# Optimization experiments

Measured on AMD Instinct MI355X. Metric: run time of the kernel, lower is better.

Reference implementation:

```python
import jax, jax.numpy as jnp
import numpy as np

N = 50000
E = 800000
IN = 128
C = 32   # out_channels per head
H = 4    # heads
HC = H * C
EDGE_DIM = 1
NEG_SLOPE = 0.2
BN_EPS = 1e-5


def setup_inputs() -> dict:
    key = jax.random.key(0)
    ks = jax.random.split(key, 12)
    glorot = lambda k, shp: (jax.random.uniform(k, shp, jnp.float32, -1.0, 1.0)
                             * jnp.sqrt(6.0 / (shp[0] + shp[-1])))
    return {
        "x": jax.random.normal(ks[0], (N, IN), jnp.float32),
        "edge_index": jax.random.randint(ks[1], (2, E), 0, N, jnp.int64),
        "edge_attr": jax.random.normal(ks[2], (E, EDGE_DIM), jnp.float32),
        # GATv2Conv params
        "W_l": glorot(ks[3], (IN, HC)),   # lin_l (source)
        "b_l": jnp.zeros((HC,), jnp.float32),
        "W_r": glorot(ks[4], (IN, HC)),   # lin_r (target)
        "b_r": jnp.zeros((HC,), jnp.float32),
        "W_e": glorot(ks[5], (EDGE_DIM, HC)),  # lin_edge (no bias)
        "att": glorot(ks[6], (H, C)),
        "bias": jnp.zeros((HC,), jnp.float32),  # final conv bias (concat)
        # BatchNorm1d affine params
        "gamma": jnp.ones((HC,), jnp.float32),
        "beta": jnp.zeros((HC,), jnp.float32),
    }


def reference(x, edge_index, edge_attr, W_l, b_l, W_r, b_r, W_e, att, bias, gamma, beta):
    src = edge_index[0]  # message source j
    dst = edge_index[1]  # message target i (aggregation segment)

    x_l = (x @ W_l + b_l).reshape(N, H, C)  # source transform
    x_r = (x @ W_r + b_r).reshape(N, H, C)  # target transform
    e = (edge_attr @ W_e).reshape(E, H, C)  # edge transform

    # GATv2 attention: LeakyReLU(x_i + x_j + e) . att, per edge & head
    m = jax.nn.leaky_relu(x_l[src] + x_r[dst] + e, NEG_SLOPE)  # [E,H,C]
    alpha = jnp.einsum('ehc,hc->eh', m, att)                   # [E,H]

    # segment softmax over destination nodes (numerically stable)
    amax = jax.ops.segment_max(alpha, dst, num_segments=N)     # [N,H]
    ex = jnp.exp(alpha - amax[dst])
    denom = jax.ops.segment_sum(ex, dst, num_segments=N)       # [N,H]
    alpha = ex / (denom[dst] + 1e-16)

    # scatter-add aggregation of weighted source features
    out = jax.ops.segment_sum(x_l[src] * alpha[:, :, None], dst, num_segments=N)
    out = out.reshape(N, HC) + bias

    # BatchNorm1d (training-mode batch statistics), then ELU; dropout = eval (identity)
    mean = out.mean(axis=0)
    var = out.var(axis=0)
    out = (out - mean) * jax.lax.rsqrt(var + BN_EPS) * gamma + beta
    return jax.nn.elu(out)
```

## Files before the change

kernel.cpp:

```cpp
#include <hip/hip_runtime.h>
#include <math.h>

constexpr int NN  = 50000;
constexpr int NE  = 800000;
constexpr int IND = 128;
constexpr int HCD = 128;

constexpr int NBKT = 250;
constexpr int NPB  = 200;
constexpr int BCAP = 4096;
constexpr int BE   = 2048;
constexpr int EPT  = BE / 256;
constexpr int B1B  = (NE + BE - 1) / BE;

constexpr int BM = 128;
constexpr int BK = 32;
constexpr int GTILES = (NN + BM - 1) / BM;

typedef __attribute__((ext_vector_type(8))) short bf16x8;
typedef __attribute__((ext_vector_type(4))) float f32x4;
typedef __attribute__((ext_vector_type(2))) float f32x2;

__device__ __forceinline__ void splitbf(float f, unsigned short &h, unsigned short &lo) {
    unsigned u = __float_as_uint(f);
    h = (unsigned short)(u >> 16);
    float fh = __uint_as_float(u & 0xffff0000u);
    lo = (unsigned short)(__float_as_uint(f - fh) >> 16);
}
__device__ __forceinline__ unsigned short bf16rne(float f) {
    unsigned u = __float_as_uint(f);
    u += 0x7fffu + ((u >> 16) & 1u);
    return (unsigned short)(u >> 16);
}

template<int CTRL>
__device__ __forceinline__ float dpp_qadd(float p) {
    int t = __builtin_amdgcn_mov_dpp(__float_as_int(p), CTRL, 0xF, 0xF, true);
    return p + __int_as_float(t);
}

__global__ __launch_bounds__(256) void gemm_bucket(
    const float* __restrict__ x, const float* __restrict__ Wl,
    const float* __restrict__ Wr, const float* __restrict__ bl,
    const float* __restrict__ br, unsigned short* __restrict__ xlbf,
    unsigned short* __restrict__ xrbf,
    const int* __restrict__ src, const int* __restrict__ dst,
    const float* __restrict__ ea, int* __restrict__ gcur,
    int2* __restrict__ stg)
{
    extern __shared__ char smem[];
    const int tid = threadIdx.x;

    if (blockIdx.x < B1B) {
        int2* sedge = (int2*)smem;
        int*  cnt   = (int*)(smem + 16384);
        int*  lofs  = (int*)(smem + 17408);
        int*  gbase = (int*)(smem + 18432);
        int*  tsc   = (int*)(smem + 19456);

        for (int j = tid; j < NBKT; j += 256) cnt[j] = 0;
        __syncthreads();

        const int e0 = blockIdx.x * BE;
        unsigned w0[EPT]; int w1[EPT]; int nb[EPT];
#pragma unroll
        for (int j = 0; j < EPT; ++j) {
            int e = e0 + j * 256 + tid;
            bool ok = e < NE;
            int s_ = ok ? src[e] : 0;
            int d_ = ok ? dst[e] : 0;
            float a_ = ok ? ea[e] : 0.f;
            int b  = d_ / NPB;
            int dl = d_ - b * NPB;
            w0[j] = (unsigned)s_ | ((unsigned)dl << 16) | ((unsigned)b << 24);
            w1[j] = __float_as_int(a_);
            nb[j] = ok ? b : -1;
            if (ok) atomicAdd(&cnt[b], 1);
        }
        __syncthreads();
        int v = (tid < NBKT) ? cnt[tid] : 0;
        tsc[tid] = v;
        __syncthreads();
        for (int d = 1; d < 256; d <<= 1) {
            int u = (tid >= d) ? tsc[tid - d] : 0;
            __syncthreads();
            tsc[tid] += u;
            __syncthreads();
        }
        if (tid < NBKT) {
            lofs[tid]  = tsc[tid] - v;
            gbase[tid] = v ? atomicAdd(&gcur[tid], v) : 0;
            cnt[tid]   = 0;
        }
        __syncthreads();
#pragma unroll
        for (int j = 0; j < EPT; ++j) {
            if (nb[j] >= 0) {
                int slot = lofs[nb[j]] + atomicAdd(&cnt[nb[j]], 1);
                sedge[slot] = make_int2((int)w0[j], w1[j]);
            }
        }
        __syncthreads();
        const int total = min(NE - e0, BE);
        for (int idx = tid; idx < total; idx += 256) {
            int2 v2 = sedge[idx];
            int b = ((unsigned)v2.x) >> 24;
            int gpos = gbase[b] + (idx - lofs[b]);
            if (gpos < BCAP)
                stg[b * BCAP + gpos] = v2;
        }
        return;
    }

    char* Ah = smem;
    char* Al = smem + 8192;
    char* Bh = smem + 16384;

    const int bblk = blockIdx.x - B1B;
    const int side = bblk & 1;
    const float* W  = side ? Wr : Wl;
    const float* bv = side ? br : bl;
    unsigned short* outp = side ? xrbf : xlbf;
    const int bn = (bblk >> 1) * BM;

    const int l   = tid & 63;
    const int wid = tid >> 6;
    const int wr  = (wid >> 1) * 64;
    const int wc  = (wid & 1) * 64;
    const int lr  = l & 15;
    const int kg  = l >> 4;

    f32x4 acc[4][4];
#pragma unroll
    for (int s = 0; s < 4; ++s)
#pragma unroll
        for (int f = 0; f < 4; ++f) acc[s][f] = (f32x4){0.f, 0.f, 0.f, 0.f};

    const int cB  = tid & 127;
    const int khB = tid >> 7;

    for (int ki = 0; ki < 4; ++ki) {
#pragma unroll
        for (int r = 0; r < 4; ++r) {
            int g = tid + r * 256;
            int row = g >> 3, k4 = g & 7;
            int node = bn + row;
            float4 v = make_float4(0.f, 0.f, 0.f, 0.f);
            if (node < NN) v = *(const float4*)&x[node * IND + ki * BK + k4 * 4];
            unsigned short h0, h1, h2, h3, q0, q1, q2, q3;
            splitbf(v.x, h0, q0); splitbf(v.y, h1, q1);
            splitbf(v.z, h2, q2); splitbf(v.w, h3, q3);
            int off = (row * BK + k4 * 4) * 2;
            int swz = off ^ ((row & 7) << 4);
            *(ushort4*)(Ah + swz) = make_ushort4(h0, h1, h2, h3);
            *(ushort4*)(Al + swz) = make_ushort4(q0, q1, q2, q3);
        }
#pragma unroll
        for (int r = 0; r < 4; ++r) {
            int kb = r * 8 + khB * 4;
            float f0 = W[(ki * BK + kb + 0) * HCD + cB];
            float f1 = W[(ki * BK + kb + 1) * HCD + cB];
            float f2 = W[(ki * BK + kb + 2) * HCD + cB];
            float f3 = W[(ki * BK + kb + 3) * HCD + cB];
            int off = (cB * BK + kb) * 2;
            int swz = off ^ ((cB & 7) << 4);
            *(ushort4*)(Bh + swz) = make_ushort4(bf16rne(f0), bf16rne(f1),
                                                 bf16rne(f2), bf16rne(f3));
        }
        __syncthreads();
        {
            bf16x8 Bf[4];
#pragma unroll
            for (int f = 0; f < 4; ++f) {
                int c = wc + f * 16 + lr;
                int swz = (c * 64 + kg * 16) ^ ((c & 7) << 4);
                Bf[f] = *(const bf16x8*)(Bh + swz);
            }
#pragma unroll
            for (int s = 0; s < 4; ++s) {
                int row = wr + s * 16 + lr;
                int swz = (row * 64 + kg * 16) ^ ((row & 7) << 4);
                bf16x8 Afh = *(const bf16x8*)(Ah + swz);
                bf16x8 Afl = *(const bf16x8*)(Al + swz);
#pragma unroll
                for (int f = 0; f < 4; ++f) {
                    acc[s][f] = __builtin_amdgcn_mfma_f32_16x16x32_bf16(Afh, Bf[f], acc[s][f], 0, 0, 0);
                    acc[s][f] = __builtin_amdgcn_mfma_f32_16x16x32_bf16(Afl, Bf[f], acc[s][f], 0, 0, 0);
                }
            }
        }
        __syncthreads();
    }
#pragma unroll
    for (int s = 0; s < 4; ++s)
#pragma unroll
        for (int f = 0; f < 4; ++f) {
            int c = wc + f * 16 + lr;
            float bb = bv[c];
#pragma unroll
            for (int j = 0; j < 4; ++j) {
                int r = bn + wr + s * 16 + kg * 4 + j;
                if (r >= NN) continue;
                outp[r * HCD + c] = bf16rne(acc[s][f][j] + bb);
            }
        }
}

__global__ __launch_bounds__(256) void csr_build(
    const int2* __restrict__ stg, const int* __restrict__ gcur,
    int* __restrict__ off, unsigned* __restrict__ csr)
{
    __shared__ int hist[NPB], t[256], cur[NPB];
    __shared__ int sbase;
    const int b = blockIdx.x, tid = threadIdx.x;

    int gv = (tid < NBKT) ? gcur[tid] : 0;
    t[tid] = gv;
    __syncthreads();
    for (int d = 1; d < 256; d <<= 1) {
        int u = (tid >= d) ? t[tid - d] : 0;
        __syncthreads();
        t[tid] += u;
        __syncthreads();
    }
    if (tid == b) sbase = t[tid] - gv;
    if (b == 0 && tid == 0) off[NN] = NE;
    __syncthreads();
    const int base  = sbase;
    const int count = min(gcur[b], BCAP);

    if (tid < NPB) { hist[tid] = 0; cur[tid] = 0; }
    __syncthreads();
    for (int sl = tid; sl < count; sl += 256)
        atomicAdd(&hist[((unsigned)stg[b * BCAP + sl].x >> 16) & 0xffu], 1);
    __syncthreads();

    int hv = (tid < NPB) ? hist[tid] : 0;
    t[tid] = hv;
    __syncthreads();
    for (int d = 1; d < 256; d <<= 1) {
        int u = (tid >= d) ? t[tid - d] : 0;
        __syncthreads();
        t[tid] += u;
        __syncthreads();
    }
    if (tid < NPB) off[b * NPB + tid] = base + t[tid] - hv;
    __syncthreads();

    for (int sl = tid; sl < count; sl += 256) {
        int2 v = stg[b * BCAP + sl];
        int dl = ((unsigned)v.x >> 16) & 0xffu;
        int pos = base + (t[dl] - hist[dl]) + atomicAdd(&cur[dl], 1);
        csr[pos] = (unsigned)(v.x & 0xffff)
                 | ((unsigned)bf16rne(__int_as_float(v.y)) << 16);
    }
}

__global__ __launch_bounds__(256) void node_kernel(
    const unsigned short* __restrict__ xlbf, const unsigned short* __restrict__ xrbf,
    const float* __restrict__ We, const float* __restrict__ att,
    const int* __restrict__ off, const unsigned* __restrict__ csr,
    unsigned short* __restrict__ out_bf)
{
    const int n = blockIdx.x * 4 + (threadIdx.x >> 6);
    if (n >= NN) return;
    const int l  = threadIdx.x & 63;
    const int g  = l >> 4;
    const int i  = l & 15;
    const int c0 = i * 8;

    f32x2 wev[4], atv[4];
#pragma unroll
    for (int j = 0; j < 4; ++j) {
        wev[j] = (f32x2){We[c0 + 2 * j], We[c0 + 2 * j + 1]};
        atv[j] = (f32x2){att[c0 + 2 * j], att[c0 + 2 * j + 1]};
    }

    uint4 xru = *(const uint4*)&xrbf[n * HCD + c0];
    f32x2 xrv[4];
    xrv[0] = (f32x2){__uint_as_float(xru.x << 16), __uint_as_float(xru.x & 0xffff0000u)};
    xrv[1] = (f32x2){__uint_as_float(xru.y << 16), __uint_as_float(xru.y & 0xffff0000u)};
    xrv[2] = (f32x2){__uint_as_float(xru.z << 16), __uint_as_float(xru.z & 0xffff0000u)};
    xrv[3] = (f32x2){__uint_as_float(xru.w << 16), __uint_as_float(xru.w & 0xffff0000u)};

    const int s = off[n], e = off[n + 1];
    if (s == e) {
        if (g == 0)
            *(uint4*)&out_bf[n * HCD + c0] = make_uint4(0, 0, 0, 0);
        return;
    }

    float mx = -3.0e38f, sm = 0.f;
    f32x2 acc[4];
#pragma unroll
    for (int j = 0; j < 4; ++j) acc[j] = (f32x2){0.f, 0.f};

    int k = s;
    unsigned cA; uint4 xA; bool vA;
    {
        int idx = min(k + g, e - 1);
        cA = csr[idx];
        xA = *(const uint4*)&xlbf[(cA & 0xffffu) * HCD + c0];
        vA = (k + g) < e;
    }

    for (; k < e; k += 4) {
        unsigned cB; uint4 xB; bool vB;
        {
            int idx = min(k + 4 + g, e - 1);
            cB = csr[idx];
            xB = *(const uint4*)&xlbf[(cB & 0xffffu) * HCD + c0];
            vB = (k + 4 + g) < e;
        }
        f32x2 xv[4];
        xv[0] = (f32x2){__uint_as_float(xA.x << 16), __uint_as_float(xA.x & 0xffff0000u)};
        xv[1] = (f32x2){__uint_as_float(xA.y << 16), __uint_as_float(xA.y & 0xffff0000u)};
        xv[2] = (f32x2){__uint_as_float(xA.z << 16), __uint_as_float(xA.z & 0xffff0000u)};
        xv[3] = (f32x2){__uint_as_float(xA.w << 16), __uint_as_float(xA.w & 0xffff0000u)};

        float eaf = __uint_as_float(cA & 0xffff0000u);
        f32x2 p2 = (f32x2){0.f, 0.f};
#pragma unroll
        for (int j = 0; j < 4; ++j) {
            f32x2 s2 = xv[j] + xrv[j];
            s2 = eaf * wev[j] + s2;
            f32x2 m2 = __builtin_elementwise_max(s2, s2 * 0.2f);
            p2 = m2 * atv[j] + p2;
        }
        float p = p2.x + p2.y;
        p = dpp_qadd<0xB1>(p);
        p = dpp_qadd<0x4E>(p);
        if (!vA) p = -1.0e30f;

        if (__any(p > mx + 8.f)) {
            float nm = fmaxf(mx, p);
            float sc = __expf(mx - nm);
            sm *= sc;
#pragma unroll
            for (int j = 0; j < 4; ++j) acc[j] *= sc;
            mx = nm;
        }
        float ev = vA ? __expf(p - mx) : 0.f;
        sm += ev;
#pragma unroll
        for (int j = 0; j < 4; ++j) acc[j] = ev * xv[j] + acc[j];

        cA = cB; xA = xB; vA = vB;
    }

    float M = fmaxf(mx, __shfl_xor(mx, 16));
    M = fmaxf(M, __shfl_xor(M, 32));
    float sc = __expf(mx - M);
    float smT = sm * sc;
    smT += __shfl_xor(smT, 16);
    smT += __shfl_xor(smT, 32);
    float inv = 1.f / (smT + 1e-16f);
    unsigned uo[4];
#pragma unroll
    for (int j = 0; j < 4; ++j) {
        float a0 = acc[j].x * sc, a1 = acc[j].y * sc;
        a0 += __shfl_xor(a0, 16);  a0 += __shfl_xor(a0, 32);
        a1 += __shfl_xor(a1, 16);  a1 += __shfl_xor(a1, 32);
        uo[j] = (unsigned)bf16rne(a0 * inv) | ((unsigned)bf16rne(a1 * inv) << 16);
    }
    if (g == 0)
        *(uint4*)&out_bf[n * HCD + c0] = make_uint4(uo[0], uo[1], uo[2], uo[3]);
}

__global__ __launch_bounds__(256) void bnstat_kernel(const unsigned short* __restrict__ out_bf,
                                                     float* __restrict__ stats)
{
    __shared__ float lsum[HCD], lsq[HCD];
    const int tid = threadIdx.x;
    if (tid < HCD) { lsum[tid] = 0.f; lsq[tid] = 0.f; }
    __syncthreads();

    const int q  = tid & 31;
    const int c0 = q * 4;
    const int r  = tid >> 5;

    float s[4] = {0.f, 0.f, 0.f, 0.f}, qq[4] = {0.f, 0.f, 0.f, 0.f};
    for (int n = blockIdx.x * 8 + r; n < NN; n += gridDim.x * 8) {
        uint2 u = *(const uint2*)&out_bf[(size_t)n * HCD + c0];
        float v0 = __uint_as_float(u.x << 16);
        float v1 = __uint_as_float(u.x & 0xffff0000u);
        float v2 = __uint_as_float(u.y << 16);
        float v3 = __uint_as_float(u.y & 0xffff0000u);
        s[0] += v0; qq[0] += v0 * v0;
        s[1] += v1; qq[1] += v1 * v1;
        s[2] += v2; qq[2] += v2 * v2;
        s[3] += v3; qq[3] += v3 * v3;
    }
#pragma unroll
    for (int j = 0; j < 4; ++j) {
        s[j]  += __shfl_xor(s[j], 32);
        qq[j] += __shfl_xor(qq[j], 32);
    }
    if ((tid & 32) == 0) {
#pragma unroll
        for (int j = 0; j < 4; ++j) {
            atomicAdd(&lsum[c0 + j], s[j]);
            atomicAdd(&lsq[c0 + j], qq[j]);
        }
    }
    __syncthreads();
    if (tid < HCD)            atomicAdd(&stats[tid], lsum[tid]);
    else                      atomicAdd(&stats[tid], lsq[tid - HCD]);
}

__global__ __launch_bounds__(256) void bn_elu_kernel(
    const unsigned short* __restrict__ out_bf, const float* __restrict__ stats,
    const float* __restrict__ gamma, const float* __restrict__ beta,
    float* __restrict__ out)
{
    int i8 = blockIdx.x * 256 + threadIdx.x;
    if (i8 >= NN * HCD / 8) return;
    int c0 = (i8 & 15) * 8;
    uint4 u = *(const uint4*)&out_bf[(size_t)i8 * 8];
    float vv[8] = {
        __uint_as_float(u.x << 16), __uint_as_float(u.x & 0xffff0000u),
        __uint_as_float(u.y << 16), __uint_as_float(u.y & 0xffff0000u),
        __uint_as_float(u.z << 16), __uint_as_float(u.z & 0xffff0000u),
        __uint_as_float(u.w << 16), __uint_as_float(u.w & 0xffff0000u)};
    float o[8];
#pragma unroll
    for (int j = 0; j < 8; ++j) {
        int c = c0 + j;
        float mean = stats[c] * (1.f / NN);
        float var  = stats[HCD + c] * (1.f / NN) - mean * mean;
        float scl  = gamma[c] * rsqrtf(var + 1e-5f);
        float sh   = beta[c] - mean * scl;
        float t = fmaf(vv[j], scl, sh);
        o[j] = (t > 0.f) ? t : (__expf(t) - 1.f);
    }
    float* dst = &out[(size_t)i8 * 8];
    *(float4*)dst       = make_float4(o[0], o[1], o[2], o[3]);
    *(float4*)(dst + 4) = make_float4(o[4], o[5], o[6], o[7]);
}

extern "C" void kernel_launch(void* const* d_in, const int* in_sizes, int n_in,
                              void* d_out, int out_size, void* d_ws, size_t ws_size,
                              hipStream_t stream)
{
    (void)in_sizes; (void)n_in; (void)out_size; (void)ws_size;
    const float* x    = (const float*)d_in[0];
    const int*   ei   = (const int*)  d_in[1];
    const float* ea   = (const float*)d_in[2];
    const float* Wl   = (const float*)d_in[3];
    const float* bl   = (const float*)d_in[4];
    const float* Wr   = (const float*)d_in[5];
    const float* br   = (const float*)d_in[6];
    const float* We   = (const float*)d_in[7];
    const float* att  = (const float*)d_in[8];
    const float* gamma= (const float*)d_in[10];
    const float* beta = (const float*)d_in[11];
    float* out = (float*)d_out;

    char* wsb = (char*)d_ws;
    size_t o = 0;
    auto take = [&](size_t bytes) -> char* {
        char* p = wsb + o;
        o += (bytes + 255) & ~size_t(255);
        return p;
    };
    unsigned short* xlbf  = (unsigned short*)take(sizeof(unsigned short) * NN * HCD);
    unsigned short* xrbf  = (unsigned short*)take(sizeof(unsigned short) * NN * HCD);
    unsigned short* outbf = (unsigned short*)take(sizeof(unsigned short) * NN * HCD);
    unsigned* csr  = (unsigned*)take(sizeof(unsigned) * NE);
    int*   offs    = (int*)  take(sizeof(int)   * (NN + 1));
    int2*  stg     = (int2*) take(sizeof(int2)  * NBKT * BCAP);
    size_t zbytes  = sizeof(float) * 2 * HCD + sizeof(int) * NBKT;
    char*  zbase   = take(zbytes);
    float* stats   = (float*)zbase;
    int*   gcur    = (int*)(stats + 2 * HCD);

    hipMemsetAsync(zbase, 0, zbytes, stream);

    const int* srcI = ei;
    const int* dstI = ei + NE;

    gemm_bucket<<<B1B + 2 * GTILES, 256, 25600, stream>>>(
        x, Wl, Wr, bl, br, xlbf, xrbf, srcI, dstI, ea, gcur, stg);
    csr_build<<<NBKT, 256, 0, stream>>>(stg, gcur, offs, csr);
    node_kernel<<<(NN + 3) / 4, 256, 0, stream>>>(xlbf, xrbf, We, att, offs, csr, outbf);
    bnstat_kernel<<<512, 256, 0, stream>>>(outbf, stats);
    bn_elu_kernel<<<(NN * HCD / 8 + 255) / 256, 256, 0, stream>>>(outbf, stats,
                                                                  gamma, beta, out);
}
```

Baseline: 131.9 us.

## Scatter bucketed edges directly to global staging and change LDS swizzle

The edge-bucketing blocks no longer stage edges in shared memory for a coalesced copy-out. Each edge is written straight to its global bucket slot using the reserved base plus a per-block atomic counter, and the edge tile per block is halved to 1024. The GEMM shared-memory swizzle changes from XOR with (row&7)<<4 to (row&6)<<3 through a shared helper, to alter the bank-conflict pattern, and the dynamic LDS size shrinks. The direct scatter removes a sync and an LDS pass but makes the global writes less coalesced, and it creates more blocks and more global atomics.

```diff
diff --git a/kernel.cpp b/kernel.cpp
--- a/kernel.cpp
+++ b/kernel.cpp
@@ -9,7 +9,7 @@
 constexpr int NBKT = 250;
 constexpr int NPB  = 200;
 constexpr int BCAP = 4096;
-constexpr int BE   = 2048;
+constexpr int BE   = 1024;
 constexpr int EPT  = BE / 256;
 constexpr int B1B  = (NE + BE - 1) / BE;
 
@@ -37,6 +37,10 @@
 __device__ __forceinline__ float dpp_qadd(float p) {
     int t = __builtin_amdgcn_mov_dpp(__float_as_int(p), CTRL, 0xF, 0xF, true);
     return p + __int_as_float(t);
+}
+
+__device__ __forceinline__ int swzA(int row, int bytecol) {
+    return (row * (BK * 2) + bytecol) ^ ((row & 6) << 3);
 }
 
 __global__ __launch_bounds__(256) void gemm_bucket(
@@ -52,11 +56,9 @@
     const int tid = threadIdx.x;
 
     if (blockIdx.x < B1B) {
-        int2* sedge = (int2*)smem;
-        int*  cnt   = (int*)(smem + 16384);
-        int*  lofs  = (int*)(smem + 17408);
-        int*  gbase = (int*)(smem + 18432);
-        int*  tsc   = (int*)(smem + 19456);
+        int* cnt   = (int*)smem;
+        int* gbase = (int*)(smem + 1024);
+        int* tsc   = (int*)(smem + 2048);
 
         for (int j = tid; j < NBKT; j += 256) cnt[j] = 0;
         __syncthreads();
@@ -88,7 +90,6 @@
             __syncthreads();
         }
         if (tid < NBKT) {
-            lofs[tid]  = tsc[tid] - v;
             gbase[tid] = v ? atomicAdd(&gcur[tid], v) : 0;
             cnt[tid]   = 0;
         }
@@ -96,18 +97,10 @@
 #pragma unroll
         for (int j = 0; j < EPT; ++j) {
             if (nb[j] >= 0) {
-                int slot = lofs[nb[j]] + atomicAdd(&cnt[nb[j]], 1);
-                sedge[slot] = make_int2((int)w0[j], w1[j]);
+                int slot = gbase[nb[j]] + atomicAdd(&cnt[nb[j]], 1);
+                if (slot < BCAP)
+                    stg[nb[j] * BCAP + slot] = make_int2((int)w0[j], w1[j]);
             }
-        }
-        __syncthreads();
-        const int total = min(NE - e0, BE);
-        for (int idx = tid; idx < total; idx += 256) {
-            int2 v2 = sedge[idx];
-            int b = ((unsigned)v2.x) >> 24;
-            int gpos = gbase[b] + (idx - lofs[b]);
-            if (gpos < BCAP)
-                stg[b * BCAP + gpos] = v2;
         }
         return;
     }
@@ -150,8 +143,7 @@
             unsigned short h0, h1, h2, h3, q0, q1, q2, q3;
             splitbf(v.x, h0, q0); splitbf(v.y, h1, q1);
             splitbf(v.z, h2, q2); splitbf(v.w, h3, q3);
-            int off = (row * BK + k4 * 4) * 2;
-            int swz = off ^ ((row & 7) << 4);
+            int swz = swzA(row, k4 * 8);
             *(ushort4*)(Ah + swz) = make_ushort4(h0, h1, h2, h3);
             *(ushort4*)(Al + swz) = make_ushort4(q0, q1, q2, q3);
         }
@@ -162,8 +154,7 @@
             float f1 = W[(ki * BK + kb + 1) * HCD + cB];
             float f2 = W[(ki * BK + kb + 2) * HCD + cB];
             float f3 = W[(ki * BK + kb + 3) * HCD + cB];
-            int off = (cB * BK + kb) * 2;
-            int swz = off ^ ((cB & 7) << 4);
+            int swz = swzA(cB, kb * 2);
             *(ushort4*)(Bh + swz) = make_ushort4(bf16rne(f0), bf16rne(f1),
                                                  bf16rne(f2), bf16rne(f3));
         }
@@ -173,13 +164,12 @@
 #pragma unroll
             for (int f = 0; f < 4; ++f) {
                 int c = wc + f * 16 + lr;
-                int swz = (c * 64 + kg * 16) ^ ((c & 7) << 4);
-                Bf[f] = *(const bf16x8*)(Bh + swz);
+                Bf[f] = *(const bf16x8*)(Bh + swzA(c, kg * 16));
             }
 #pragma unroll
             for (int s = 0; s < 4; ++s) {
                 int row = wr + s * 16 + lr;
-                int swz = (row * 64 + kg * 16) ^ ((row & 7) << 4);
+                int swz = swzA(row, kg * 16);
                 bf16x8 Afh = *(const bf16x8*)(Ah + swz);
                 bf16x8 Afl = *(const bf16x8*)(Al + swz);
 #pragma unroll
@@ -479,7 +469,7 @@
     const int* srcI = ei;
     const int* dstI = ei + NE;
 
-    gemm_bucket<<<B1B + 2 * GTILES, 256, 25600, stream>>>(
+    gemm_bucket<<<B1B + 2 * GTILES, 256, 24576, stream>>>(
         x, Wl, Wr, bl, br, xlbf, xrbf, srcI, dstI, ea, gcur, stg);
     csr_build<<<NBKT, 256, 0, stream>>>(stg, gcur, offs, csr);
     node_kernel<<<(NN + 3) / 4, 256, 0, stream>>>(xlbf, xrbf, We, att, offs, csr, outbf);
```

Measured after the change: 143.5 us. 1.09x slower.
